# Kernel optimization log

Hardware: AMD Instinct MI355X
Metric: run time of the kernel (lower is better)

The kernel has to match this reference:

```python
import jax, jax.numpy as jnp
import numpy as np

D_MODEL, D_STATE, D_CONV, D_INNER = 1024, 16, 4, 2048
BATCH, SEQ = 2, 2048


def setup_inputs() -> dict:
    key = jax.random.key(0)
    ks = jax.random.split(key, 12)
    s = 0.02
    inp = {
        "x": jax.random.normal(ks[0], (BATCH, SEQ, D_MODEL), jnp.float32),
        # Linear weights stored (in, out): y = x @ W + b (equivalent to torch x @ W.T + b)
        "W_in": jax.random.normal(ks[1], (D_MODEL, 2 * D_INNER), jnp.float32) * s,
        "b_in": jnp.zeros((2 * D_INNER,), jnp.float32),
        # depthwise conv kernel (OIH) with groups=d_inner -> (d_inner, 1, d_conv)
        "conv_w": jax.random.normal(ks[2], (D_INNER, 1, D_CONV), jnp.float32) * s,
        "conv_b": jnp.zeros((D_INNER,), jnp.float32),
        "W_x": jax.random.normal(ks[3], (D_INNER, 2 * D_STATE), jnp.float32) * s,
        "b_x": jnp.zeros((2 * D_STATE,), jnp.float32),
        "W_dt": jax.random.normal(ks[4], (D_INNER, D_INNER), jnp.float32) * s,
        "b_dt": jnp.zeros((D_INNER,), jnp.float32),
        # A_log init: log(arange(1..d_state)) tiled over d_inner, as in the module
        "A_log": jnp.log(jnp.tile(jnp.arange(1, D_STATE + 1, dtype=jnp.float32), (D_INNER, 1))),
        "D": jnp.ones((D_INNER,), jnp.float32),
        "W_out": jax.random.normal(ks[5], (D_INNER, D_MODEL), jnp.float32) * s,
        "b_out": jnp.zeros((D_MODEL,), jnp.float32),
    }
    return inp


def reference(x, W_in, b_in, conv_w, conv_b, W_x, b_x, W_dt, b_dt, A_log, D, W_out, b_out):
    d_inner, d_state = A_log.shape
    d_conv = conv_w.shape[-1]
    bsz, seq_len, _ = x.shape

    xz = x @ W_in + b_in                      # (B, L, 2*Din)
    xh, z = jnp.split(xz, 2, axis=-1)

    # causal depthwise conv: torch pads both sides by d_conv-1 then slices [:L]
    # == left-pad-only causal conv
    xc = jnp.transpose(xh, (0, 2, 1))         # (B, Din, L)
    xc = jax.lax.conv_general_dilated(
        xc, conv_w, window_strides=(1,), padding=[(d_conv - 1, 0)],
        dimension_numbers=("NCH", "OIH", "NCH"), feature_group_count=d_inner)
    xc = xc + conv_b[None, :, None]
    xh = jax.nn.silu(jnp.transpose(xc, (0, 2, 1)))  # (B, L, Din)

    A = -jnp.exp(A_log)                       # (Din, N)
    x_dbl = xh @ W_x + b_x                    # (B, L, 2N)
    Bmat = x_dbl[..., d_state:]               # second chunk; first chunk is discarded
    delta = jax.nn.softplus(xh @ W_dt + b_dt) # (B, L, Din)

    def step(h, inp):
        d_t, b_t, u_t = inp                    # (B,Din), (B,N), (B,Din)
        dA = jnp.exp(d_t[:, :, None] * A)      # (B, Din, N)
        dBu = d_t[:, :, None] * b_t[:, None, :] * u_t[:, :, None]
        h = dA * h + dBu
        return h, h.sum(-1)                    # y_t: (B, Din)

    h0 = jnp.zeros((bsz, d_inner, d_state), x.dtype)
    _, ys = jax.lax.scan(step, h0, (jnp.swapaxes(delta, 0, 1),
                                    jnp.swapaxes(Bmat, 0, 1),
                                    jnp.swapaxes(xh, 0, 1)))
    y = jnp.swapaxes(ys, 0, 1) + xh * D       # skip connection with D
    y = y * jax.nn.silu(z)                    # gate
    return y @ W_out + b_out                  # (B, L, d_model)
```

## Files before the change

kernel.cpp:

```cpp
#include <hip/hip_runtime.h>
#include <stdint.h>

#define NDM   1024
#define NDS   16
#define NDC   4
#define NDI   2048
#define NB    2
#define NL    2048
#define MROWS (NB*NL)
#define CCH   32
#define CLEN  64

typedef __bf16 bf16x8 __attribute__((ext_vector_type(8)));
typedef float  f32x4  __attribute__((ext_vector_type(4)));
typedef short  short8 __attribute__((ext_vector_type(8)));

__device__ __forceinline__ short f2bf(float f) {
  union { float f; unsigned u; } x; x.f = f;
  unsigned r = (x.u + 0x7FFFu + ((x.u >> 16) & 1u)) >> 16;
  return (short)r;
}
__device__ __forceinline__ float bf2f(short s) {
  union { unsigned u; float f; } x; x.u = ((unsigned)(unsigned short)s) << 16;
  return x.f;
}

__device__ __forceinline__ size_t fgoff(int row, int k8, int K) {
  return (size_t)(row >> 4) * K * 16 + (size_t)k8 * 128 + (row & 15) * 8;
}

__global__ __launch_bounds__(256) void cvt_fg_kernel(
    const float* __restrict__ in, short* __restrict__ out) {
  __shared__ short slab[16][1032];
  const int tid = threadIdx.x;
  const int g = blockIdx.x;
  const float* p = in + (size_t)g * 16 * 1024;
  #pragma unroll
  for (int u = 0; u < 8; ++u) {
    int unit = u * 256 + tid;
    int rr = unit >> 7, cc = unit & 127;
    const float* rp = p + (size_t)rr * 1024 + cc * 8;
    #pragma unroll
    for (int e = 0; e < 8; ++e) slab[rr][cc * 8 + e] = f2bf(rp[e]);
  }
  __syncthreads();
  short* op = out + (size_t)g * 16384;
  #pragma unroll
  for (int u = 0; u < 8; ++u) {
    int u2 = u * 256 + tid;
    int rr = u2 & 15, k8 = u2 >> 4;
    *(short8*)&op[k8 * 128 + rr * 8] = *(short8*)&slab[rr][k8 * 8];
  }
}

__global__ __launch_bounds__(256) void transpose_fg_kernel(
    const float* __restrict__ in, short* __restrict__ out, int K, int N) {
  __shared__ float t[64][33];
  const int tx = threadIdx.x, ty = threadIdx.y;
  const int n0 = blockIdx.x * 32, k0 = blockIdx.y * 64;
  #pragma unroll
  for (int i = 0; i < 64; i += 8)
    t[ty + i][tx] = in[(size_t)(k0 + ty + i) * N + n0 + tx];
  __syncthreads();
  const int n = n0 + tx, k8 = (k0 >> 3) + ty;
  short8 v;
  #pragma unroll
  for (int e = 0; e < 8; ++e) v[e] = f2bf(t[ty * 8 + e][tx]);
  *(short8*)&out[fgoff(n, k8, K)] = v;
}

__global__ __launch_bounds__(256) void wx_fg_kernel(
    const float* __restrict__ Wx, short* __restrict__ Wcat) {
  int t = blockIdx.x * 256 + threadIdx.x;
  int k8 = t >> 4, n = t & 15;
  short8 v;
  #pragma unroll
  for (int e = 0; e < 8; ++e)
    v[e] = f2bf(Wx[(size_t)(k8 * 8 + e) * (2 * NDS) + NDS + n]);
  *(short8*)&Wcat[(size_t)128 * 2048 * 16 + (size_t)k8 * 128 + n * 8] = v;
}

template<int BN, int EPI>
__global__ __launch_bounds__(256, 2) void gemm_fg_kernel(
    const short* __restrict__ A, const short* __restrict__ Bt,
    const float* __restrict__ bias, float* __restrict__ C,
    short* __restrict__ Cb, float* __restrict__ Bm,
    const float* __restrict__ bx, int M, int N, int K)
{
  const int tid  = threadIdx.x;
  const int lane = tid & 63;
  const int w    = tid >> 6;
  const int wM   = w >> 1;
  const int wN   = w & 1;
  const int g    = lane >> 4;
  const int r    = lane & 15;

  constexpr int FN  = BN / 32;
  constexpr int CTS = BN + 8;
  __shared__ short ctile_s[(EPI == 0) ? 2 : 128 * CTS];

  const int nx  = gridDim.x;
  const int nwg = nx * gridDim.y;
  const int bid = blockIdx.y * nx + blockIdx.x;
  const int swz = (bid & 7) * (nwg >> 3) + (bid >> 3);
  const int bm  = (swz / nx) * 128;
  const int bn  = (swz % nx) * BN;

  const short* pA[4];
  const short* pB[FN];
  #pragma unroll
  for (int m = 0; m < 4; ++m)
    pA[m] = A + (size_t)((bm >> 4) + wM * 4 + m) * K * 16 + lane * 8;
  #pragma unroll
  for (int n = 0; n < FN; ++n)
    pB[n] = Bt + (size_t)((bn >> 4) + wN * FN + n) * K * 16 + lane * 8;

  f32x4 acc[4][FN];
  #pragma unroll
  for (int m = 0; m < 4; ++m)
    #pragma unroll
    for (int n = 0; n < FN; ++n)
      acc[m][n] = (f32x4){0.f, 0.f, 0.f, 0.f};

  bf16x8 a0[4], b0[FN], a1[4], b1[FN];
  #pragma unroll
  for (int m = 0; m < 4; ++m) a0[m] = *(const bf16x8*)(pA[m]);
  #pragma unroll
  for (int n = 0; n < FN; ++n) b0[n] = *(const bf16x8*)(pB[n]);

  for (int kb = 0; kb < K; kb += 64) {
    if (kb + 32 < K) {
      #pragma unroll
      for (int m = 0; m < 4; ++m)
        a1[m] = *(const bf16x8*)(pA[m] + (size_t)(kb + 32) * 16);
      #pragma unroll
      for (int n = 0; n < FN; ++n)
        b1[n] = *(const bf16x8*)(pB[n] + (size_t)(kb + 32) * 16);
    }
    #pragma unroll
    for (int m = 0; m < 4; ++m)
      #pragma unroll
      for (int n = 0; n < FN; ++n)
        acc[m][n] = __builtin_amdgcn_mfma_f32_16x16x32_bf16(
            a0[m], b0[n], acc[m][n], 0, 0, 0);

    if (kb + 64 < K) {
      #pragma unroll
      for (int m = 0; m < 4; ++m)
        a0[m] = *(const bf16x8*)(pA[m] + (size_t)(kb + 64) * 16);
      #pragma unroll
      for (int n = 0; n < FN; ++n)
        b0[n] = *(const bf16x8*)(pB[n] + (size_t)(kb + 64) * 16);
    }
    #pragma unroll
    for (int m = 0; m < 4; ++m)
      #pragma unroll
      for (int n = 0; n < FN; ++n)
        acc[m][n] = __builtin_amdgcn_mfma_f32_16x16x32_bf16(
            a1[m], b1[n], acc[m][n], 0, 0, 0);
  }

  if constexpr (EPI == 2) {
    short (*ctile)[CTS] = (short(*)[CTS])ctile_s;
    #pragma unroll
    for (int m = 0; m < 4; ++m) {
      const int rl0 = wM * 64 + m * 16 + g * 4;
      #pragma unroll
      for (int n = 0; n < FN; ++n) {
        const int cl = wN * (BN / 2) + n * 16 + r;
        const float bv = bias[bn + cl];
        #pragma unroll
        for (int e = 0; e < 4; ++e)
          ctile[rl0 + e][cl] = f2bf(acc[m][n][e] + bv);
      }
    }
    __syncthreads();
    #pragma unroll
    for (int it = 0; it < (128 * BN / 8) / 256; ++it) {
      int id = it * 256 + tid;
      int rowL = id / (BN / 8), c8 = id % (BN / 8);
      *(short8*)&Cb[(size_t)(bm + rowL) * N + bn + c8 * 8] =
          *(short8*)&ctile[rowL][c8 * 8];
    }
  } else if constexpr (EPI == 1) {
    short (*ctile)[CTS] = (short(*)[CTS])ctile_s;
    #pragma unroll
    for (int m = 0; m < 4; ++m) {
      const int rl0 = wM * 64 + m * 16 + g * 4;
      const int row0 = bm + rl0;
      #pragma unroll
      for (int n = 0; n < FN; ++n) {
        const int colbase = bn + wN * (BN / 2) + n * 16;
        if (colbase < 2048) {
          const int cl = wN * (BN / 2) + n * 16 + r;
          const float bv = bias[colbase + r];
          #pragma unroll
          for (int e = 0; e < 4; ++e) {
            float v = acc[m][n][e] + bv;
            v = (v > 15.f) ? v : log1pf(__expf(v));
            ctile[rl0 + e][cl] = f2bf(v);
          }
        } else if (colbase == 2048) {
          const float bv = bx[NDS + r];
          #pragma unroll
          for (int e = 0; e < 4; ++e)
            Bm[(size_t)(row0 + e) * NDS + r] = acc[m][n][e] + bv;
        }
      }
    }
    __syncthreads();
    if (bn < 2048) {
      constexpr int CH = 2 * BN;
      #pragma unroll
      for (int it = 0; it < (8 * CH) / 256; ++it) {
        int unit = it * 256 + tid;
        int grp = unit / CH, wi = unit % CH;
        int k8l = wi >> 4, rr = wi & 15;
        *(short8*)&Cb[(size_t)((bm >> 4) + grp) * (NDI * 16) +
                      (size_t)((bn >> 3) + k8l) * 128 + rr * 8] =
            *(short8*)&ctile[grp * 16 + rr][k8l * 8];
      }
    }
  } else {
    #pragma unroll
    for (int m = 0; m < 4; ++m) {
      const int row0 = bm + wM * 64 + m * 16 + g * 4;
      #pragma unroll
      for (int n = 0; n < FN; ++n) {
        const int col = bn + wN * (BN / 2) + n * 16 + r;
        const float bv = bias[col];
        #pragma unroll
        for (int e = 0; e < 4; ++e)
          C[(size_t)(row0 + e) * N + col] = acc[m][n][e] + bv;
      }
    }
  }
}

__global__ __launch_bounds__(256) void conv_silu_kernel(
    const short* __restrict__ xz, const float* __restrict__ cw,
    const float* __restrict__ cb, short* __restrict__ xhbf) {
  __shared__ short slab[16][528];
  const int tid = threadIdx.x;
  const int c0 = blockIdx.x * 512;
  const int r0 = blockIdx.y * 16;
  const int b  = r0 >> 11;
  const int t0 = r0 & (NL - 1);
  const short* zbase = xz + ((size_t)b * NL) * (2 * NDI);

  #pragma unroll
  for (int u = 0; u < 4; ++u) {
    int unit = u * 256 + tid;
    int rr = unit >> 6, cc = unit & 63;
    int t = t0 + rr, c = c0 + cc * 8;
    float acc[8];
    #pragma unroll
    for (int e = 0; e < 8; ++e) acc[e] = cb[c + e];
    #pragma unroll
    for (int k = 0; k < NDC; ++k) {
      int tt = t - (NDC - 1) + k;
      if (tt >= 0) {
        short8 rv = *(const short8*)(zbase + (size_t)tt * (2 * NDI) + c);
        #pragma unroll
        for (int e = 0; e < 8; ++e)
          acc[e] += cw[(c + e) * NDC + k] * bf2f(rv[e]);
      }
    }
    #pragma unroll
    for (int e = 0; e < 8; ++e) {
      float s = acc[e] / (1.f + __expf(-acc[e]));
      slab[rr][cc * 8 + e] = f2bf(s);
    }
  }
  __syncthreads();
  short* op = xhbf + (size_t)(r0 >> 4) * NDI * 16 + (size_t)(c0 >> 3) * 128;
  #pragma unroll
  for (int u = 0; u < 4; ++u) {
    int u2 = u * 256 + tid;
    int rr = u2 & 15, q = u2 >> 4;
    *(short8*)&op[q * 128 + rr * 8] = *(short8*)&slab[rr][q * 8];
  }
}

__device__ __forceinline__ size_t scoff(int b, int k, int c) {
  return (((size_t)b * CCH + k) * NDI + c) * NDS;
}

__global__ __launch_bounds__(256) void scan_p1_kernel(
    const short* __restrict__ dbf, const float* __restrict__ Bm,
    const short* __restrict__ xhbf, const float* __restrict__ A_log,
    float* __restrict__ Pbuf, float* __restrict__ Hend) {
  const int i = blockIdx.x * 256 + threadIdx.x;
  const int c = i & (NDI - 1);
  const int k = (i >> 11) & (CCH - 1);
  const int b = i >> 16;
  const int t0 = k * CLEN;

  float Av[NDS];
  #pragma unroll
  for (int s = 0; s < NDS; ++s) Av[s] = -__expf(A_log[c * NDS + s]);

  const size_t fgb = (size_t)((b * NL + t0) >> 4) * (NDI * 16) +
                     (size_t)(c >> 3) * 128 + (c & 7);
  const short* up = xhbf + fgb;
  const short* dp = dbf + fgb;
  const f32x4* Bp = (const f32x4*)(Bm + ((size_t)(b * NL + t0)) * NDS);

  float h[NDS], P[NDS];
  #pragma unroll
  for (int s = 0; s < NDS; ++s) { h[s] = 0.f; P[s] = 1.f; }

  #pragma unroll 4
  for (int j = 0; j < CLEN; ++j) {
    const size_t o = (size_t)(j >> 4) * (NDI * 16) + (j & 15) * 8;
    const float d = bf2f(dp[o]);
    const float u = bf2f(up[o]);
    f32x4 B0 = Bp[j * 4 + 0], B1 = Bp[j * 4 + 1];
    f32x4 B2 = Bp[j * 4 + 2], B3 = Bp[j * 4 + 3];
    const float du = d * u;
    float Bv[NDS];
    #pragma unroll
    for (int e = 0; e < 4; ++e) {
      Bv[e] = B0[e]; Bv[4 + e] = B1[e]; Bv[8 + e] = B2[e]; Bv[12 + e] = B3[e];
    }
    #pragma unroll
    for (int s = 0; s < NDS; ++s) {
      float dA = __expf(d * Av[s]);
      h[s] = dA * h[s] + du * Bv[s];
      P[s] *= dA;
    }
  }

  const size_t base = scoff(b, k, c);
  #pragma unroll
  for (int q = 0; q < 4; ++q) {
    *(f32x4*)&Pbuf[base + q * 4] = (f32x4){P[q*4], P[q*4+1], P[q*4+2], P[q*4+3]};
    *(f32x4*)&Hend[base + q * 4] = (f32x4){h[q*4], h[q*4+1], h[q*4+2], h[q*4+3]};
  }
}

__global__ __launch_bounds__(256) void scan_p2_kernel(
    const float* __restrict__ Pbuf, const float* __restrict__ Hend,
    float* __restrict__ Hin) {
  const int i = blockIdx.x * 256 + threadIdx.x;
  const int s = i & (NDS - 1);
  const int c = (i >> 4) & (NDI - 1);
  const int b = i >> 15;
  const size_t step = (size_t)NDI * NDS;
  const size_t base = scoff(b, 0, c) + s;
  float h = 0.f;
  #pragma unroll 8
  for (int k = 0; k < CCH; ++k) {
    Hin[base + (size_t)k * step] = h;
    h = Hend[base + (size_t)k * step] + Pbuf[base + (size_t)k * step] * h;
  }
}

__global__ __launch_bounds__(256) void scan_p3_kernel(
    const short* __restrict__ dbf, const float* __restrict__ Bm,
    const short* __restrict__ xhbf, const float* __restrict__ A_log,
    const float* __restrict__ Hin, const float* __restrict__ Dvec,
    const short* __restrict__ xz, short* __restrict__ ybf) {
  const int tid = threadIdx.x;
  const int i = blockIdx.x * 256 + tid;
  const int c = i & (NDI - 1);
  const int k = (i >> 11) & (CCH - 1);
  const int b = i >> 16;
  const int t0 = k * CLEN;
  const int cb0 = (blockIdx.x * 256) & (NDI - 1);

  __shared__ float ylds[16][257];

  float Av[NDS];
  #pragma unroll
  for (int s = 0; s < NDS; ++s) Av[s] = -__expf(A_log[c * NDS + s]);
  const float dcoef = Dvec[c];

  const size_t fgb = (size_t)((b * NL + t0) >> 4) * (NDI * 16) +
                     (size_t)(c >> 3) * 128 + (c & 7);
  const short* up = xhbf + fgb;
  const short* dp = dbf + fgb;
  const f32x4* Bp = (const f32x4*)(Bm + ((size_t)(b * NL + t0)) * NDS);
  const short* zp = xz + ((size_t)(b * NL + t0)) * (2 * NDI) + NDI + c;

  const size_t base = scoff(b, k, c);
  float h[NDS];
  #pragma unroll
  for (int s = 0; s < NDS; ++s) h[s] = Hin[base + s];

  for (int j = 0; j < CLEN; ++j) {
    const size_t o = (size_t)(j >> 4) * (NDI * 16) + (j & 15) * 8;
    const float d = bf2f(dp[o]);
    const float u = bf2f(up[o]);
    f32x4 B0 = Bp[j * 4 + 0], B1 = Bp[j * 4 + 1];
    f32x4 B2 = Bp[j * 4 + 2], B3 = Bp[j * 4 + 3];
    const float du = d * u;
    float Bv[NDS];
    #pragma unroll
    for (int e = 0; e < 4; ++e) {
      Bv[e] = B0[e]; Bv[4 + e] = B1[e]; Bv[8 + e] = B2[e]; Bv[12 + e] = B3[e];
    }
    #pragma unroll
    for (int s = 0; s < NDS; ++s) {
      float dA = __expf(d * Av[s]);
      h[s] = dA * h[s] + du * Bv[s];
    }
    float sum01 = 0.f, sum23 = 0.f;
    #pragma unroll
    for (int s = 0; s < 8; ++s)  sum01 += h[s];
    #pragma unroll
    for (int s = 8; s < 16; ++s) sum23 += h[s];
    float y = sum01 + sum23 + u * dcoef;
    float z = bf2f(zp[(size_t)j * (2 * NDI)]);
    y *= z / (1.f + __expf(-z));
    ylds[j & 15][tid] = y;

    if ((j & 15) == 15) {
      __syncthreads();
      const int jb = j - 15;
      #pragma unroll
      for (int s2 = 0; s2 < 2; ++s2) {
        int u2 = tid + 256 * s2;
        int tt = u2 & 15, q = u2 >> 4;
        short8 v;
        #pragma unroll
        for (int e = 0; e < 8; ++e) v[e] = f2bf(ylds[tt][q * 8 + e]);
        int grow = b * NL + t0 + jb + tt;
        int k8 = (cb0 >> 3) + q;
        *(short8*)&ybf[fgoff(grow, k8, NDI)] = v;
      }
      __syncthreads();
    }
  }
}

extern "C" void kernel_launch(void* const* d_in, const int* in_sizes, int n_in,
                              void* d_out, int out_size, void* d_ws, size_t ws_size,
                              hipStream_t stream) {
  const float* x      = (const float*)d_in[0];
  const float* W_in   = (const float*)d_in[1];
  const float* b_in   = (const float*)d_in[2];
  const float* conv_w = (const float*)d_in[3];
  const float* conv_b = (const float*)d_in[4];
  const float* W_x    = (const float*)d_in[5];
  const float* b_x    = (const float*)d_in[6];
  const float* W_dt   = (const float*)d_in[7];
  const float* b_dt   = (const float*)d_in[8];
  const float* A_log  = (const float*)d_in[9];
  const float* Dv     = (const float*)d_in[10];
  const float* W_out  = (const float*)d_in[11];
  const float* b_out  = (const float*)d_in[12];
  float* out = (float*)d_out;

  char* w = (char*)d_ws;
  short* xbf   = (short*)(w);
  short* WtIn  = (short*)(w + 8388608);
  short* WtCat = (short*)(w + 16777216);
  short* WtOut = (short*)(w + 25690112);
  short* xzbf  = (short*)(w + 29884416);
  short* xhbf  = (short*)(w + 96993280);
  short* dbf   = (short*)(w + 113770496);
  float* Bm    = (float*)(w + 147324928);
  short* ybf   = (short*)(w + 147587072);
  float* Pbuf  = (float*)(w);
  float* Hend  = (float*)(w + 8388608);
  float* Hin   = (float*)(w + 16777216);

  hipMemsetAsync((char*)WtCat + (size_t)129 * 65536, 0, 7 * 65536, stream);

  cvt_fg_kernel<<<MROWS / 16, 256, 0, stream>>>(x, xbf);
  transpose_fg_kernel<<<dim3((2 * NDI) / 32, NDM / 64), dim3(32, 8), 0, stream>>>(
      W_in, WtIn, NDM, 2 * NDI);
  transpose_fg_kernel<<<dim3(NDI / 32, NDI / 64), dim3(32, 8), 0, stream>>>(
      W_dt, WtCat, NDI, NDI);
  wx_fg_kernel<<<16, 256, 0, stream>>>(W_x, WtCat);
  transpose_fg_kernel<<<dim3(NDM / 32, NDI / 64), dim3(32, 8), 0, stream>>>(
      W_out, WtOut, NDI, NDM);

  gemm_fg_kernel<64, 2><<<dim3((2 * NDI) / 64, MROWS / 128), 256, 0, stream>>>(
      xbf, WtIn, b_in, nullptr, xzbf, nullptr, nullptr,
      MROWS, 2 * NDI, NDM);

  conv_silu_kernel<<<dim3(NDI / 512, MROWS / 16), 256, 0, stream>>>(
      xzbf, conv_w, conv_b, xhbf);

  gemm_fg_kernel<64, 1><<<dim3(2176 / 64, MROWS / 128), 256, 0, stream>>>(
      xhbf, WtCat, b_dt, nullptr, dbf, Bm, b_x,
      MROWS, NDI, NDI);

  scan_p1_kernel<<<(NB * NDI * CCH) / 256, 256, 0, stream>>>(
      dbf, Bm, xhbf, A_log, Pbuf, Hend);
  scan_p2_kernel<<<(NB * NDI * NDS) / 256, 256, 0, stream>>>(Pbuf, Hend, Hin);
  scan_p3_kernel<<<(NB * NDI * CCH) / 256, 256, 0, stream>>>(
      dbf, Bm, xhbf, A_log, Hin, Dv, xzbf, ybf);

  gemm_fg_kernel<64, 0><<<dim3(NDM / 64, MROWS / 128), 256, 0, stream>>>(
      ybf, WtOut, b_out, out, nullptr, nullptr, nullptr,
      MROWS, NDM, NDI);
}
```

Baseline: 336.9 us.

## Stage GEMM tiles through LDS with async triple-buffered global_load_lds pipeline

The GEMM kernel previously loaded A and B fragments directly from global memory into registers. It now copies them asynchronously into LDS using global_load_lds, triple-buffered, with vmcnt waits and barriers, and raises MFMA priority during compute. The first two GEMMs also move to 128-wide N tiles and occupancy is bumped to 3 waves per SIMD. The aim is to hide global latency and share loaded tiles across waves, at the cost of more LDS use and a barrier per k-step. The 2176-column GEMM yields 17 column tiles, and the swizzle, which assumes the block count is divisible by 8, may not map blocks cleanly.

New measurement: 319.5 us. 1.05x faster.

```diff
diff --git a/kernel.cpp b/kernel.cpp
--- a/kernel.cpp
+++ b/kernel.cpp
@@ -29,6 +29,13 @@
   return (size_t)(row >> 4) * K * 16 + (size_t)k8 * 128 + (row & 15) * 8;
 }
 
+__device__ __forceinline__ void gload16(const void* g, void* l) {
+  __builtin_amdgcn_global_load_lds(
+      (__attribute__((address_space(1))) void*)(uintptr_t)g,
+      (__attribute__((address_space(3))) void*)l,
+      16, 0, 0);
+}
+
 __global__ __launch_bounds__(256) void cvt_fg_kernel(
     const float* __restrict__ in, short* __restrict__ out) {
   __shared__ short slab[16][1032];
@@ -81,7 +88,7 @@
 }
 
 template<int BN, int EPI>
-__global__ __launch_bounds__(256, 2) void gemm_fg_kernel(
+__global__ __launch_bounds__(256, 3) void gemm_fg_kernel(
     const short* __restrict__ A, const short* __restrict__ Bt,
     const float* __restrict__ bias, float* __restrict__ C,
     short* __restrict__ Cb, float* __restrict__ Bm,
@@ -95,9 +102,13 @@
   const int g    = lane >> 4;
   const int r    = lane & 15;
 
-  constexpr int FN  = BN / 32;
-  constexpr int CTS = BN + 8;
-  __shared__ short ctile_s[(EPI == 0) ? 2 : 128 * CTS];
+  constexpr int FN   = BN / 32;
+  constexpr int BTS  = BN * 32;
+  constexpr int SLOT = 4096 + BTS;
+  constexpr int STG  = 3 * SLOT;
+  constexpr int CTS  = BN + 8;
+  constexpr int POOL = (EPI != 0 && STG < 128 * CTS) ? 128 * CTS : STG;
+  __shared__ short pool[POOL];
 
   const int nx  = gridDim.x;
   const int nwg = nx * gridDim.y;
@@ -106,14 +117,36 @@
   const int bm  = (swz / nx) * 128;
   const int bn  = (swz % nx) * BN;
 
-  const short* pA[4];
-  const short* pB[FN];
-  #pragma unroll
-  for (int m = 0; m < 4; ++m)
-    pA[m] = A + (size_t)((bm >> 4) + wM * 4 + m) * K * 16 + lane * 8;
-  #pragma unroll
-  for (int n = 0; n < FN; ++n)
-    pB[n] = Bt + (size_t)((bn >> 4) + wN * FN + n) * K * 16 + lane * 8;
+  const short* pA[2];
+  #pragma unroll
+  for (int q = 0; q < 2; ++q)
+    pA[q] = A + (size_t)((bm >> 4) + 2 * w + q) * K * 16 + lane * 8;
+  const short* pB[2];
+  if constexpr (BN == 128) {
+    #pragma unroll
+    for (int q = 0; q < 2; ++q)
+      pB[q] = Bt + (size_t)((bn >> 4) + 2 * w + q) * K * 16 + lane * 8;
+  } else {
+    pB[0] = Bt + (size_t)((bn >> 4) + w) * K * 16 + lane * 8;
+    pB[1] = pB[0];
+  }
+
+#define STAGE(buf, kb)                                                      \
+  do {                                                                      \
+    _Pragma("unroll")                                                       \
+    for (int q = 0; q < 2; ++q)                                             \
+      gload16(pA[q] + (size_t)(kb) * 16,                                    \
+              pool + (buf) * SLOT + (2 * w + q) * 512);                     \
+    if constexpr (BN == 128) {                                              \
+      _Pragma("unroll")                                                     \
+      for (int q = 0; q < 2; ++q)                                           \
+        gload16(pB[q] + (size_t)(kb) * 16,                                  \
+                pool + (buf) * SLOT + 4096 + (2 * w + q) * 512);            \
+    } else {                                                                \
+      gload16(pB[0] + (size_t)(kb) * 16,                                    \
+              pool + (buf) * SLOT + 4096 + w * 512);                        \
+    }                                                                       \
+  } while (0)
 
   f32x4 acc[4][FN];
   #pragma unroll
@@ -122,46 +155,46 @@
     for (int n = 0; n < FN; ++n)
       acc[m][n] = (f32x4){0.f, 0.f, 0.f, 0.f};
 
-  bf16x8 a0[4], b0[FN], a1[4], b1[FN];
-  #pragma unroll
-  for (int m = 0; m < 4; ++m) a0[m] = *(const bf16x8*)(pA[m]);
-  #pragma unroll
-  for (int n = 0; n < FN; ++n) b0[n] = *(const bf16x8*)(pB[n]);
-
-  for (int kb = 0; kb < K; kb += 64) {
-    if (kb + 32 < K) {
-      #pragma unroll
-      for (int m = 0; m < 4; ++m)
-        a1[m] = *(const bf16x8*)(pA[m] + (size_t)(kb + 32) * 16);
-      #pragma unroll
-      for (int n = 0; n < FN; ++n)
-        b1[n] = *(const bf16x8*)(pB[n] + (size_t)(kb + 32) * 16);
-    }
+  const int NT = K >> 5;
+  STAGE(0, 0);
+  STAGE(1, 32);
+  int cur = 0;
+  for (int t = 0; t < NT; ++t) {
+    if (t < NT - 1) {
+      if constexpr (BN == 128)
+        asm volatile("s_waitcnt vmcnt(4)" ::: "memory");
+      else
+        asm volatile("s_waitcnt vmcnt(3)" ::: "memory");
+    } else {
+      asm volatile("s_waitcnt vmcnt(0)" ::: "memory");
+    }
+    __builtin_amdgcn_s_barrier();
+    __builtin_amdgcn_sched_barrier(0);
+    if (t + 2 < NT) STAGE((t + 2) % 3, (t + 2) * 32);
+
+    bf16x8 af[4], bfv[FN];
+    #pragma unroll
+    for (int m = 0; m < 4; ++m)
+      af[m] = *(const bf16x8*)(pool + cur * SLOT + (wM * 4 + m) * 512 + lane * 8);
+    #pragma unroll
+    for (int n = 0; n < FN; ++n)
+      bfv[n] = *(const bf16x8*)(pool + cur * SLOT + 4096 +
+                                (wN * FN + n) * 512 + lane * 8);
+    __builtin_amdgcn_s_setprio(1);
     #pragma unroll
     for (int m = 0; m < 4; ++m)
       #pragma unroll
       for (int n = 0; n < FN; ++n)
         acc[m][n] = __builtin_amdgcn_mfma_f32_16x16x32_bf16(
-            a0[m], b0[n], acc[m][n], 0, 0, 0);
-
-    if (kb + 64 < K) {
-      #pragma unroll
-      for (int m = 0; m < 4; ++m)
-        a0[m] = *(const bf16x8*)(pA[m] + (size_t)(kb + 64) * 16);
-      #pragma unroll
-      for (int n = 0; n < FN; ++n)
-        b0[n] = *(const bf16x8*)(pB[n] + (size_t)(kb + 64) * 16);
-    }
-    #pragma unroll
-    for (int m = 0; m < 4; ++m)
-      #pragma unroll
-      for (int n = 0; n < FN; ++n)
-        acc[m][n] = __builtin_amdgcn_mfma_f32_16x16x32_bf16(
-            a1[m], b1[n], acc[m][n], 0, 0, 0);
-  }
+            af[m], bfv[n], acc[m][n], 0, 0, 0);
+    __builtin_amdgcn_s_setprio(0);
+    cur = (cur + 1 == 3) ? 0 : cur + 1;
+  }
+#undef STAGE
 
   if constexpr (EPI == 2) {
-    short (*ctile)[CTS] = (short(*)[CTS])ctile_s;
+    __syncthreads();
+    short (*ctile)[CTS] = (short(*)[CTS])pool;
     #pragma unroll
     for (int m = 0; m < 4; ++m) {
       const int rl0 = wM * 64 + m * 16 + g * 4;
@@ -183,7 +216,8 @@
           *(short8*)&ctile[rowL][c8 * 8];
     }
   } else if constexpr (EPI == 1) {
-    short (*ctile)[CTS] = (short(*)[CTS])ctile_s;
+    __syncthreads();
+    short (*ctile)[CTS] = (short(*)[CTS])pool;
     #pragma unroll
     for (int m = 0; m < 4; ++m) {
       const int rl0 = wM * 64 + m * 16 + g * 4;
@@ -477,14 +511,14 @@
   transpose_fg_kernel<<<dim3(NDM / 32, NDI / 64), dim3(32, 8), 0, stream>>>(
       W_out, WtOut, NDI, NDM);
 
-  gemm_fg_kernel<64, 2><<<dim3((2 * NDI) / 64, MROWS / 128), 256, 0, stream>>>(
+  gemm_fg_kernel<128, 2><<<dim3((2 * NDI) / 128, MROWS / 128), 256, 0, stream>>>(
       xbf, WtIn, b_in, nullptr, xzbf, nullptr, nullptr,
       MROWS, 2 * NDI, NDM);
 
   conv_silu_kernel<<<dim3(NDI / 512, MROWS / 16), 256, 0, stream>>>(
       xzbf, conv_w, conv_b, xhbf);
 
-  gemm_fg_kernel<64, 1><<<dim3(2176 / 64, MROWS / 128), 256, 0, stream>>>(
+  gemm_fg_kernel<128, 1><<<dim3(2176 / 128, MROWS / 128), 256, 0, stream>>>(
       xhbf, WtCat, b_dt, nullptr, dbf, Bm, b_x,
       MROWS, NDI, NDI);
 
```
